# Optimization experiments

Measured on AMD Instinct MI355X. Metric: run time of the kernel, lower is better.

The kernel has to match this reference:

```python
import jax, jax.numpy as jnp
import numpy as np

MODEL_DIM = 256
PAIR_IMPORTANCE_WEIGHT = 0.5
B, S, D = 4, 4096, MODEL_DIM


def setup_inputs() -> dict:
    key = jax.random.key(0)
    ks = jax.random.split(key, 6)
    return {
        "query": jax.random.normal(ks[0], (B, S, D), dtype=jnp.float32),
        "key": jax.random.normal(ks[1], (B, S, D), dtype=jnp.float32),
        "value": jax.random.normal(ks[2], (B, S, D), dtype=jnp.float32),
        "W_query": jax.random.normal(ks[3], (D, D), dtype=jnp.float32),
        "W_key": jax.random.normal(ks[4], (D, D), dtype=jnp.float32),
        "W_value": jax.random.normal(ks[5], (D, D), dtype=jnp.float32),
    }


def reference(query, key, value, W_query, W_key, W_value):
    # Projections: [B,S,D] @ [D,D]
    q = jnp.einsum('bsd,de->bse', query, W_query)
    k = jnp.einsum('bsd,de->bse', key, W_key)
    v = jnp.einsum('bsd,de->bse', value, W_value)
    scale = jnp.sqrt(jnp.asarray(MODEL_DIM, dtype=q.dtype))
    # Full [B,S,S] score matrix (global max forces materialization)
    scores = jnp.einsum('bqd,bkd->bqk', q, k) / scale
    s_len = scores.shape[1]
    diag_bias = jnp.eye(s_len, dtype=scores.dtype) * jnp.max(scores)
    scores = scores + PAIR_IMPORTANCE_WEIGHT * diag_bias  # broadcast over batch
    attention_weights = jax.nn.softmax(scores, axis=-1)
    output = jnp.einsum('bqk,bkd->bqd', attention_weights, v)
    return output, attention_weights
```

## Files before the change

kernel.cpp:

```cpp
#include <hip/hip_runtime.h>
#include <cstdint>
#include <cstddef>

#define BB 4
#define SS 4096
#define DD 256
#define SCORE_SCALE (1.0f/16.0f)
#define PIW 0.5f
#define NROWS (BB * SS)

typedef float          f32x4  __attribute__((ext_vector_type(4)));
typedef __bf16         bf16v8 __attribute__((ext_vector_type(8)));
typedef unsigned short u16v8  __attribute__((ext_vector_type(8)));
typedef unsigned short u16v4  __attribute__((ext_vector_type(4)));

__device__ __forceinline__ f32x4 mfma_bf16(u16v8 a, u16v8 b, f32x4 c) {
    return __builtin_amdgcn_mfma_f32_16x16x32_bf16(
        __builtin_bit_cast(bf16v8, a), __builtin_bit_cast(bf16v8, b), c, 0, 0, 0);
}

__device__ __forceinline__ unsigned short f2bf(float f) {
    unsigned u = __float_as_uint(f);
    u += 0x7FFFu + ((u >> 16) & 1u);
    return (unsigned short)(u >> 16);
}
__device__ __forceinline__ float bf2f(unsigned short h) {
    return __uint_as_float(((unsigned)h) << 16);
}
__device__ __forceinline__ unsigned fenc(float x) {
    unsigned u = __float_as_uint(x);
    return (u & 0x80000000u) ? ~u : (u | 0x80000000u);
}
__device__ __forceinline__ float fdec(unsigned e) {
    return __uint_as_float((e & 0x80000000u) ? (e ^ 0x80000000u) : ~e);
}

#define PSPAD 42

__global__ __launch_bounds__(256) void proj_kernel(
    const float* __restrict__ query, const float* __restrict__ key_, const float* __restrict__ value,
    const float* __restrict__ Wq, const float* __restrict__ Wk, const float* __restrict__ Wv,
    unsigned short* __restrict__ qh, unsigned short* __restrict__ ql,
    unsigned short* __restrict__ kh, unsigned short* __restrict__ kl,
    unsigned short* __restrict__ vT, unsigned* __restrict__ gmax)
{
    const int z = blockIdx.z;
    const float* A = (z == 0) ? query : (z == 1) ? key_ : value;
    const float* W = (z == 0) ? Wq    : (z == 1) ? Wk   : Wv;
    if (z == 0 && blockIdx.x == 0 && blockIdx.y == 0 && threadIdx.x == 0)
        *gmax = 0x007FFFFFu;

    __shared__ unsigned short Ah[128][PSPAD];
    __shared__ unsigned short Al[128][PSPAD];
    __shared__ unsigned short Bh[128][PSPAD];
    __shared__ unsigned short Bl[128][PSPAD];

    const int tid = threadIdx.x;
    const int lane = tid & 63, w = tid >> 6;
    const int wr = (w >> 1) * 64, wc = (w & 1) * 64;
    const int m = lane & 15, qq = lane >> 4;
    const int rowBase = blockIdx.y * 128;
    const int colBase = blockIdx.x * 128;

    f32x4 acc[4][4];
    #pragma unroll
    for (int i = 0; i < 4; i++)
        #pragma unroll
        for (int j = 0; j < 4; j++)
            acc[i][j] = (f32x4){0.f, 0.f, 0.f, 0.f};

    const int chunk = (tid & 3) * 8;
    const int srow  = tid >> 2;

    for (int k0 = 0; k0 < DD; k0 += 32) {
        #pragma unroll
        for (int i = 0; i < 2; i++) {
            int r = srow + i * 64;
            const float* src = &A[(size_t)(rowBase + r) * DD + k0 + chunk];
            float4 f0 = *(const float4*)src;
            float4 f1 = *(const float4*)(src + 4);
            float v[8] = {f0.x, f0.y, f0.z, f0.w, f1.x, f1.y, f1.z, f1.w};
            u16v8 h, l;
            #pragma unroll
            for (int e = 0; e < 8; e++) {
                h[e] = f2bf(v[e]);
                l[e] = f2bf(v[e] - bf2f(h[e]));
            }
            *(u16v8*)&Ah[r][chunk] = h;
            *(u16v8*)&Al[r][chunk] = l;
        }
        #pragma unroll
        for (int i = 0; i < 4; i++) {
            int idx = tid + i * 256;
            int kk = idx >> 5, nq = idx & 31;
            float4 f = *(const float4*)&W[(size_t)(k0 + kk) * DD + colBase + nq * 4];
            float v[4] = {f.x, f.y, f.z, f.w};
            #pragma unroll
            for (int e = 0; e < 4; e++) {
                unsigned short h = f2bf(v[e]);
                unsigned short l = f2bf(v[e] - bf2f(h));
                Bh[nq * 4 + e][kk] = h;
                Bl[nq * 4 + e][kk] = l;
            }
        }
        __syncthreads();

        const int kb = qq * 8;
        u16v8 ah[4], al[4], bh[4], bl[4];
        #pragma unroll
        for (int i = 0; i < 4; i++) {
            ah[i] = *(const u16v8*)&Ah[wr + i * 16 + m][kb];
            al[i] = *(const u16v8*)&Al[wr + i * 16 + m][kb];
            bh[i] = *(const u16v8*)&Bh[wc + i * 16 + m][kb];
            bl[i] = *(const u16v8*)&Bl[wc + i * 16 + m][kb];
        }
        #pragma unroll
        for (int i = 0; i < 4; i++)
            #pragma unroll
            for (int j = 0; j < 4; j++) {
                acc[i][j] = mfma_bf16(ah[i], bh[j], acc[i][j]);
                acc[i][j] = mfma_bf16(ah[i], bl[j], acc[i][j]);
                acc[i][j] = mfma_bf16(al[i], bh[j], acc[i][j]);
            }
        __syncthreads();
    }

    #pragma unroll
    for (int i = 0; i < 4; i++) {
        #pragma unroll
        for (int j = 0; j < 4; j++) {
            #pragma unroll
            for (int r = 0; r < 4; r++) {
                const int gr  = rowBase + wr + i * 16 + qq * 4 + r;
                const int col = colBase + wc + j * 16 + m;
                const float v = acc[i][j][r];
                if (z == 2) {
                    const int b2 = gr >> 12, s2 = gr & (SS - 1);
                    vT[((size_t)b2 * DD + col) * SS + s2] = f2bf(v);
                } else {
                    unsigned short h = f2bf(v);
                    unsigned short l = f2bf(v - bf2f(h));
                    unsigned short* H = (z == 0) ? qh : kh;
                    unsigned short* L = (z == 0) ? ql : kl;
                    H[(size_t)gr * DD + col] = h;
                    L[(size_t)gr * DD + col] = l;
                }
            }
        }
    }
}

#define SPAD 40

__global__ __launch_bounds__(256) void scores_mfma(
    const unsigned short* __restrict__ qh, const unsigned short* __restrict__ ql,
    const unsigned short* __restrict__ kh, const unsigned short* __restrict__ kl,
    float* __restrict__ attn, unsigned* __restrict__ gmax,
    float* __restrict__ tmaxg, float* __restrict__ tsumg)
{
    const int b = blockIdx.z;
    const size_t boff = (size_t)b * SS * DD;
    const unsigned short* Qh = qh + boff;
    const unsigned short* Ql = ql + boff;
    const unsigned short* Kh = kh + boff;
    const unsigned short* Kl = kl + boff;
    float* C = attn + (size_t)b * SS * SS;

    __shared__ unsigned short Ah[128][SPAD];
    __shared__ unsigned short Al[128][SPAD];
    __shared__ unsigned short Bh[128][SPAD];
    __shared__ unsigned short Bl[128][SPAD];
    __shared__ float s_m[4][64];
    __shared__ float s_s[4][64];
    __shared__ float red[128];

    const int tid = threadIdx.x;
    const int lane = tid & 63, w = tid >> 6;
    const int wr = (w >> 1) * 64, wc = (w & 1) * 64;
    const int m = lane & 15, qq = lane >> 4;
    const int rowBase = blockIdx.y * 128;
    const int colBase = blockIdx.x * 128;

    f32x4 acc[4][4];
    #pragma unroll
    for (int i = 0; i < 4; i++)
        #pragma unroll
        for (int j = 0; j < 4; j++)
            acc[i][j] = (f32x4){0.f, 0.f, 0.f, 0.f};

    const int chunk = (tid & 3) * 8;
    const int srow  = tid >> 2;

    for (int k0 = 0; k0 < DD; k0 += 32) {
        #pragma unroll
        for (int i = 0; i < 2; i++) {
            int r = srow + i * 64;
            size_t ga = (size_t)(rowBase + r) * DD + k0 + chunk;
            size_t gb = (size_t)(colBase + r) * DD + k0 + chunk;
            *(u16v8*)&Ah[r][chunk] = *(const u16v8*)&Qh[ga];
            *(u16v8*)&Al[r][chunk] = *(const u16v8*)&Ql[ga];
            *(u16v8*)&Bh[r][chunk] = *(const u16v8*)&Kh[gb];
            *(u16v8*)&Bl[r][chunk] = *(const u16v8*)&Kl[gb];
        }
        __syncthreads();

        const int kb = qq * 8;
        u16v8 ah[4], al[4], bh[4], bl[4];
        #pragma unroll
        for (int i = 0; i < 4; i++) {
            ah[i] = *(const u16v8*)&Ah[wr + i * 16 + m][kb];
            al[i] = *(const u16v8*)&Al[wr + i * 16 + m][kb];
            bh[i] = *(const u16v8*)&Bh[wc + i * 16 + m][kb];
            bl[i] = *(const u16v8*)&Bl[wc + i * 16 + m][kb];
        }
        #pragma unroll
        for (int i = 0; i < 4; i++)
            #pragma unroll
            for (int j = 0; j < 4; j++) {
                acc[i][j] = mfma_bf16(ah[i], bh[j], acc[i][j]);
                acc[i][j] = mfma_bf16(ah[i], bl[j], acc[i][j]);
                acc[i][j] = mfma_bf16(al[i], bh[j], acc[i][j]);
            }
        __syncthreads();
    }

    #pragma unroll
    for (int i = 0; i < 4; i++)
        #pragma unroll
        for (int j = 0; j < 4; j++)
            acc[i][j] *= SCORE_SCALE;

    #pragma unroll
    for (int i = 0; i < 4; i++)
        #pragma unroll
        for (int j = 0; j < 4; j++)
            #pragma unroll
            for (int r = 0; r < 4; r++) {
                int row = rowBase + wr + i * 16 + qq * 4 + r;
                int col = colBase + wc + j * 16 + m;
                __builtin_nontemporal_store(acc[i][j][r], &C[(size_t)row * SS + col]);
            }

    float lmax[16];
    #pragma unroll
    for (int i = 0; i < 4; i++)
        #pragma unroll
        for (int r = 0; r < 4; r++)
            lmax[i * 4 + r] = fmaxf(fmaxf(acc[i][0][r], acc[i][1][r]),
                                    fmaxf(acc[i][2][r], acc[i][3][r]));
    #pragma unroll
    for (int t = 0; t < 16; t++) {
        #pragma unroll
        for (int msk = 1; msk < 16; msk <<= 1)
            lmax[t] = fmaxf(lmax[t], __shfl_xor(lmax[t], msk));
    }
    if (m == 0) {
        #pragma unroll
        for (int i = 0; i < 4; i++)
            #pragma unroll
            for (int r = 0; r < 4; r++)
                s_m[w][i * 16 + qq * 4 + r] = lmax[i * 4 + r];
    }
    __syncthreads();
    float lsum[16];
    #pragma unroll
    for (int i = 0; i < 4; i++)
        #pragma unroll
        for (int r = 0; r < 4; r++) {
            int idx = i * 16 + qq * 4 + r;
            float rm = fmaxf(s_m[w][idx], s_m[w ^ 1][idx]);
            float s = 0.f;
            #pragma unroll
            for (int j = 0; j < 4; j++)
                s += __expf(acc[i][j][r] - rm);
            lsum[i * 4 + r] = s;
        }
    #pragma unroll
    for (int t = 0; t < 16; t++) {
        #pragma unroll
        for (int msk = 1; msk < 16; msk <<= 1)
            lsum[t] += __shfl_xor(lsum[t], msk);
    }
    if (m == 0) {
        #pragma unroll
        for (int i = 0; i < 4; i++)
            #pragma unroll
            for (int r = 0; r < 4; r++)
                s_s[w][i * 16 + qq * 4 + r] = lsum[i * 4 + r];
    }
    __syncthreads();

    if (tid < 128) {
        int wp = tid >> 6, lr = tid & 63;
        float tm = fmaxf(s_m[2 * wp][lr], s_m[2 * wp + 1][lr]);
        float ts = s_s[2 * wp][lr] + s_s[2 * wp + 1][lr];
        size_t gi = (size_t)blockIdx.x * NROWS + (size_t)b * SS + rowBase + tid;
        tmaxg[gi] = tm;
        tsumg[gi] = ts;
        red[tid] = tm;
    }
    __syncthreads();
    for (int s2 = 64; s2 > 0; s2 >>= 1) {
        if (tid < s2) red[tid] = fmaxf(red[tid], red[tid + s2]);
        __syncthreads();
    }
    if (tid == 0) atomicMax(gmax, fenc(red[0]));
}

__global__ __launch_bounds__(256) void stats_merge(
    const float* __restrict__ tmaxg, const float* __restrict__ tsumg,
    const float* __restrict__ attn, const unsigned* __restrict__ gmax,
    float* __restrict__ rowm, float* __restrict__ rowinv)
{
    const int grow = blockIdx.x * 256 + threadIdx.x;
    const int b = grow >> 12, i = grow & (SS - 1);
    const float bias = PIW * fdec(*gmax);

    float tm[32];
    float mx = -INFINITY;
    #pragma unroll
    for (int t = 0; t < 32; t++) {
        tm[t] = tmaxg[(size_t)t * NROWS + grow];
        mx = fmaxf(mx, tm[t]);
    }
    const float dii = attn[(size_t)b * SS * SS + (size_t)i * SS + i];
    mx = fmaxf(mx, dii + bias);

    float s = 0.f;
    #pragma unroll
    for (int t = 0; t < 32; t++)
        s += tsumg[(size_t)t * NROWS + grow] * __expf(tm[t] - mx);
    s += __expf(dii + bias - mx) - __expf(dii - mx);

    rowm[grow] = mx;
    rowinv[grow] = 1.0f / s;
}

#define AVBK 256

__global__ __launch_bounds__(256) void av_softmax_mfma(
    float* __restrict__ attn, const unsigned short* __restrict__ vT,
    const float* __restrict__ rowm, const float* __restrict__ rowinv,
    const unsigned* __restrict__ gmax, float* __restrict__ out)
{
    const int lin = blockIdx.x;
    const int b = (lin & 7) >> 1;
    const int rowTile = ((lin >> 3) << 1) | (lin & 1);
    const int rowBase = rowTile * 32;

    float* A = attn + (size_t)b * SS * SS;
    const unsigned short* Bv = vT + (size_t)b * DD * SS;
    const float bias = PIW * fdec(*gmax);

    __shared__ unsigned short As[2][32][264];

    const int tid = threadIdx.x;
    const int lane = tid & 63, w = tid >> 6;
    const int m = lane & 15, qq = lane >> 4;

    const int ra = tid >> 3;
    const int c8 = tid & 7;
    const int rr = rowBase + ra;
    float* Arow = A + (size_t)rr * SS;
    const float mr = rowm[b * SS + rr];
    const float ri = rowinv[b * SS + rr];

    const unsigned short* Bp[4];
    #pragma unroll
    for (int j = 0; j < 4; j++)
        Bp[j] = Bv + (size_t)(w * 64 + j * 16 + m) * SS;

    f32x4 acc[2][4];
    #pragma unroll
    for (int i = 0; i < 2; i++)
        #pragma unroll
        for (int j = 0; j < 4; j++)
            acc[i][j] = (f32x4){0.f, 0.f, 0.f, 0.f};

    f32x4 pf[8];

    auto loadA = [&](int kbase) {
        #pragma unroll
        for (int u = 0; u < 8; u++)
            pf[u] = *(const f32x4*)&Arow[kbase + c8 * 4 + u * 32];
    };
    auto procStore = [&](int kbase, int buf) {
        #pragma unroll
        for (int u = 0; u < 8; u++) {
            int c = c8 * 4 + u * 32;
            int j0 = kbase + c;
            float e0 = pf[u][0] + ((j0 + 0 == rr) ? bias : 0.0f);
            float e1 = pf[u][1] + ((j0 + 1 == rr) ? bias : 0.0f);
            float e2 = pf[u][2] + ((j0 + 2 == rr) ? bias : 0.0f);
            float e3 = pf[u][3] + ((j0 + 3 == rr) ? bias : 0.0f);
            float w0 = __expf(e0 - mr) * ri;
            float w1 = __expf(e1 - mr) * ri;
            float w2 = __expf(e2 - mr) * ri;
            float w3 = __expf(e3 - mr) * ri;
            f32x4 wv = (f32x4){w0, w1, w2, w3};
            __builtin_nontemporal_store(wv, (f32x4*)&Arow[j0]);
            *(u16v4*)&As[buf][ra][c] =
                (u16v4){f2bf(w0), f2bf(w1), f2bf(w2), f2bf(w3)};
        }
    };

    const int NT = SS / AVBK;

    loadA(0);
    procStore(0, 0);
    __syncthreads();

    for (int t = 0; t < NT; t++) {
        const int k0 = t * AVBK;
        const int cur = t & 1;
        if (t + 1 < NT)
            loadA(k0 + AVBK);
        #pragma unroll
        for (int kk = 0; kk < 8; kk++) {
            const int kb = kk * 32 + qq * 8;
            u16v8 bf_[4], af_[2];
            #pragma unroll
            for (int j = 0; j < 4; j++)
                bf_[j] = *(const u16v8*)&Bp[j][k0 + kb];
            #pragma unroll
            for (int i = 0; i < 2; i++)
                af_[i] = *(const u16v8*)&As[cur][i * 16 + m][kb];
            #pragma unroll
            for (int i = 0; i < 2; i++)
                #pragma unroll
                for (int j = 0; j < 4; j++)
                    acc[i][j] = mfma_bf16(af_[i], bf_[j], acc[i][j]);
        }
        if (t + 1 < NT) {
            procStore(k0 + AVBK, cur ^ 1);
            __syncthreads();
        }
    }

    #pragma unroll
    for (int i = 0; i < 2; i++) {
        #pragma unroll
        for (int j = 0; j < 4; j++) {
            #pragma unroll
            for (int r = 0; r < 4; r++) {
                int row = rowBase + i * 16 + qq * 4 + r;
                int col = w * 64 + j * 16 + m;
                __builtin_nontemporal_store(
                    acc[i][j][r], &out[((size_t)b * SS + row) * DD + col]);
            }
        }
    }
}

extern "C" void kernel_launch(void* const* d_in, const int* in_sizes, int n_in,
                              void* d_out, int out_size, void* d_ws, size_t ws_size,
                              hipStream_t stream)
{
    const float* query = (const float*)d_in[0];
    const float* key_  = (const float*)d_in[1];
    const float* value = (const float*)d_in[2];
    const float* Wq    = (const float*)d_in[3];
    const float* Wk    = (const float*)d_in[4];
    const float* Wv    = (const float*)d_in[5];

    float* out  = (float*)d_out;
    float* attn = out + (size_t)BB * SS * DD;

    const size_t E = (size_t)BB * SS * DD;
    unsigned short* qh = (unsigned short*)d_ws;
    unsigned short* ql = qh + E;
    unsigned short* kh = ql + E;
    unsigned short* kl = kh + E;
    unsigned short* vT = kl + E;
    float* tmaxg  = (float*)(vT + E);
    float* tsumg  = tmaxg + 32 * (size_t)NROWS;
    float* rowm   = tsumg + 32 * (size_t)NROWS;
    float* rowinv = rowm + NROWS;
    unsigned* gmax = (unsigned*)(rowinv + NROWS);

    proj_kernel<<<dim3(DD / 128, (BB * SS) / 128, 3), 256, 0, stream>>>(
        query, key_, value, Wq, Wk, Wv, qh, ql, kh, kl, vT, gmax);
    scores_mfma<<<dim3(SS / 128, SS / 128, BB), 256, 0, stream>>>(
        qh, ql, kh, kl, attn, gmax, tmaxg, tsumg);
    stats_merge<<<dim3(NROWS / 256), 256, 0, stream>>>(
        tmaxg, tsumg, attn, gmax, rowm, rowinv);
    av_softmax_mfma<<<dim3(512), 256, 0, stream>>>(
        attn, vT, rowm, rowinv, gmax, out);
}
```

Baseline: 656.0 us.

## Split AV softmax kernel over key halves and add partial-output reduction

The attention-times-V kernel now splits the key dimension in two, doubling the grid from 512 to 1024 blocks. Each block writes a partial output into workspace that reuses the now-dead projection buffers, and a new reduce kernel sums the two halves. The aim is better occupancy and latency hiding across the CUs, at the cost of an extra launch and extra partial-output traffic. Separately, the scores kernel now writes its score tile after the max reduction and the atomic update rather than before, which may overlap the stores with other work.

```diff
diff --git a/kernel.cpp b/kernel.cpp
--- a/kernel.cpp
+++ b/kernel.cpp
@@ -230,17 +230,6 @@
         for (int j = 0; j < 4; j++)
             acc[i][j] *= SCORE_SCALE;
 
-    #pragma unroll
-    for (int i = 0; i < 4; i++)
-        #pragma unroll
-        for (int j = 0; j < 4; j++)
-            #pragma unroll
-            for (int r = 0; r < 4; r++) {
-                int row = rowBase + wr + i * 16 + qq * 4 + r;
-                int col = colBase + wc + j * 16 + m;
-                __builtin_nontemporal_store(acc[i][j][r], &C[(size_t)row * SS + col]);
-            }
-
     float lmax[16];
     #pragma unroll
     for (int i = 0; i < 4; i++)
@@ -305,6 +294,17 @@
         __syncthreads();
     }
     if (tid == 0) atomicMax(gmax, fenc(red[0]));
+
+    #pragma unroll
+    for (int i = 0; i < 4; i++)
+        #pragma unroll
+        for (int j = 0; j < 4; j++)
+            #pragma unroll
+            for (int r = 0; r < 4; r++) {
+                int row = rowBase + wr + i * 16 + qq * 4 + r;
+                int col = colBase + wc + j * 16 + m;
+                __builtin_nontemporal_store(acc[i][j][r], &C[(size_t)row * SS + col]);
+            }
 }
 
 __global__ __launch_bounds__(256) void stats_merge(
@@ -341,12 +341,14 @@
 __global__ __launch_bounds__(256) void av_softmax_mfma(
     float* __restrict__ attn, const unsigned short* __restrict__ vT,
     const float* __restrict__ rowm, const float* __restrict__ rowinv,
-    const unsigned* __restrict__ gmax, float* __restrict__ out)
+    const unsigned* __restrict__ gmax, float* __restrict__ outp)
 {
     const int lin = blockIdx.x;
     const int b = (lin & 7) >> 1;
-    const int rowTile = ((lin >> 3) << 1) | (lin & 1);
+    const int khalf = lin & 1;
+    const int rowTile = lin >> 3;
     const int rowBase = rowTile * 32;
+    const int kq0 = khalf * (SS / 2);
 
     float* A = attn + (size_t)b * SS * SS;
     const unsigned short* Bv = vT + (size_t)b * DD * SS;
@@ -404,14 +406,14 @@
         }
     };
 
-    const int NT = SS / AVBK;
-
-    loadA(0);
-    procStore(0, 0);
+    const int NT = (SS / 2) / AVBK;
+
+    loadA(kq0);
+    procStore(kq0, 0);
     __syncthreads();
 
     for (int t = 0; t < NT; t++) {
-        const int k0 = t * AVBK;
+        const int k0 = kq0 + t * AVBK;
         const int cur = t & 1;
         if (t + 1 < NT)
             loadA(k0 + AVBK);
@@ -437,6 +439,7 @@
         }
     }
 
+    float* OP = outp + (size_t)khalf * BB * SS * DD;
     #pragma unroll
     for (int i = 0; i < 2; i++) {
         #pragma unroll
@@ -445,11 +448,20 @@
             for (int r = 0; r < 4; r++) {
                 int row = rowBase + i * 16 + qq * 4 + r;
                 int col = w * 64 + j * 16 + m;
-                __builtin_nontemporal_store(
-                    acc[i][j][r], &out[((size_t)b * SS + row) * DD + col]);
-            }
-        }
-    }
+                OP[((size_t)b * SS + row) * DD + col] = acc[i][j][r];
+            }
+        }
+    }
+}
+
+__global__ __launch_bounds__(256) void reduce_out(
+    const float* __restrict__ outp, float* __restrict__ out)
+{
+    const size_t i = ((size_t)blockIdx.x * 256 + threadIdx.x) * 4;
+    f32x4 a = *(const f32x4*)&outp[i];
+    f32x4 c = *(const f32x4*)&outp[(size_t)BB * SS * DD + i];
+    f32x4 s = a + c;
+    __builtin_nontemporal_store(s, (f32x4*)&out[i]);
 }
 
 extern "C" void kernel_launch(void* const* d_in, const int* in_sizes, int n_in,
@@ -477,6 +489,7 @@
     float* rowm   = tsumg + 32 * (size_t)NROWS;
     float* rowinv = rowm + NROWS;
     unsigned* gmax = (unsigned*)(rowinv + NROWS);
+    float* outp = (float*)d_ws;
 
     proj_kernel<<<dim3(DD / 128, (BB * SS) / 128, 3), 256, 0, stream>>>(
         query, key_, value, Wq, Wk, Wv, qh, ql, kh, kl, vT, gmax);
@@ -484,6 +497,7 @@
         qh, ql, kh, kl, attn, gmax, tmaxg, tsumg);
     stats_merge<<<dim3(NROWS / 256), 256, 0, stream>>>(
         tmaxg, tsumg, attn, gmax, rowm, rowinv);
-    av_softmax_mfma<<<dim3(512), 256, 0, stream>>>(
-        attn, vT, rowm, rowinv, gmax, out);
-}
+    av_softmax_mfma<<<dim3(1024), 256, 0, stream>>>(
+        attn, vT, rowm, rowinv, gmax, outp);
+    reduce_out<<<dim3((int)(E / 1024)), 256, 0, stream>>>(outp, out);
+}
```

Result: no change. 666.7 us (+1.6%).
